# Performance work log

Measured on AMD Instinct MI355X. Metric: run time of the kernel, lower is better.

## Reference

```python
import jax, jax.numpy as jnp
import numpy as np

B, T, D, H, L = 4, 2048, 256, 4, 2
HD = D // H
VOCAB, MAX_BITS, MLP_H = 32, 64, 64


def setup_inputs() -> dict:
    key = jax.random.key(0)
    ks = jax.random.split(key, 20)
    s = 0.02
    n = lambda k, shp: (jax.random.normal(k, shp, jnp.float32) * s)
    inp = {
        'tokens': jax.random.randint(ks[0], (B, T), 0, VOCAB),
        'embed': n(ks[1], (VOCAB, D)),
        'ln1_w': jnp.ones((L, D)), 'ln1_b': jnp.zeros((L, D)),
        'qkv_w': n(ks[2], (L, D, 3 * D)), 'qkv_b': jnp.zeros((L, 3 * D)),
        'proj_w': n(ks[3], (L, D, D)), 'proj_b': jnp.zeros((L, D)),
        'ln2_w': jnp.ones((L, D)), 'ln2_b': jnp.zeros((L, D)),
        'ffn1_w': n(ks[4], (L, D, 4 * D)), 'ffn1_b': jnp.zeros((L, 4 * D)),
        'ffn2_w': n(ks[5], (L, 4 * D, D)), 'ffn2_b': jnp.zeros((L, D)),
        'lnf_w': jnp.ones((D,)), 'lnf_b': jnp.zeros((D,)),
        'out_queries': n(ks[6], (MAX_BITS * 2, D)),
        'outp_w': n(ks[7], (D, 1)), 'outp_b': jnp.zeros((1,)),
        'mlp_w1': n(ks[8], (3, MLP_H)), 'mlp_b1': jnp.zeros((MLP_H,)),
        'mlp_w2': n(ks[9], (MLP_H, MLP_H)), 'mlp_b2': jnp.zeros((MLP_H,)),
        'mlp_w3': n(ks[10], (MLP_H, 2)), 'mlp_b3': jnp.zeros((2,)),
    }
    return inp


def _layernorm(x, w, b, eps=1e-5):
    mu = jnp.mean(x, axis=-1, keepdims=True)
    var = jnp.mean(jnp.square(x - mu), axis=-1, keepdims=True)
    return (x - mu) * jax.lax.rsqrt(var + eps) * w + b


def _rope_tables(t_len, hd):
    inv_freq = 1.0 / (10000.0 ** (jnp.arange(0, hd, 2, dtype=jnp.float32) / hd))
    freqs = jnp.outer(jnp.arange(t_len, dtype=jnp.float32), inv_freq)  # [T, hd/2]
    emb = jnp.concatenate([freqs, freqs], axis=-1)                     # [T, hd]
    return jnp.cos(emb)[None, :, None, :], jnp.sin(emb)[None, :, None, :]


def _rotate_half(x):
    x1, x2 = x[..., : x.shape[-1] // 2], x[..., x.shape[-1] // 2:]
    return jnp.concatenate([-x2, x1], axis=-1)


def _attention(x, qkv_w, qkv_b, proj_w, proj_b):
    b, t, c = x.shape
    qkv = (x @ qkv_w + qkv_b).reshape(b, t, 3, H, HD)
    q, k, v = qkv[:, :, 0], qkv[:, :, 1], qkv[:, :, 2]  # [B,T,H,HD]
    cos, sin = _rope_tables(t, HD)
    q = q * cos + _rotate_half(q) * sin
    k = k * cos + _rotate_half(k) * sin
    scores = jnp.einsum('bthd,bshd->bhts', q, k) / jnp.sqrt(jnp.float32(HD))
    causal = jnp.tril(jnp.ones((t, t), dtype=bool))
    scores = jnp.where(causal, scores, -jnp.inf)
    attn = jax.nn.softmax(scores, axis=-1)
    out = jnp.einsum('bhts,bshd->bthd', attn, v).reshape(b, t, c)
    return out @ proj_w + proj_b


def reference(tokens, embed, ln1_w, ln1_b, qkv_w, qkv_b, proj_w, proj_b,
              ln2_w, ln2_b, ffn1_w, ffn1_b, ffn2_w, ffn2_b, lnf_w, lnf_b,
              out_queries, outp_w, outp_b,
              mlp_w1, mlp_b1, mlp_w2, mlp_b2, mlp_w3, mlp_b3):
    x = embed[tokens]  # [B,T,D]
    for l in range(L):
        x = x + _attention(_layernorm(x, ln1_w[l], ln1_b[l]),
                           qkv_w[l], qkv_b[l], proj_w[l], proj_b[l])
        h = _layernorm(x, ln2_w[l], ln2_b[l])
        h = jax.nn.gelu(h @ ffn1_w[l] + ffn1_b[l], approximate=False)
        x = x + (h @ ffn2_w[l] + ffn2_b[l])
    x = _layernorm(x, lnf_w, lnf_b)
    # query cross-attention for bit-pair selection
    q_scores = jnp.einsum('qd,btd->bqt', out_queries, x) / jnp.sqrt(jnp.float32(D))
    q_attn = jax.nn.softmax(q_scores, axis=-1)           # [B, 2*MAX_BITS, T]
    selected = jnp.einsum('bqt,btd->bqd', q_attn, x)
    bits = jax.nn.sigmoid((selected @ outp_w + outp_b)[..., 0])
    pairs = bits.reshape(-1, MAX_BITS, 2)                # [B, MAX_BITS, 2]

    # sequential full-adder over bits
    def step(carry, ab):  # carry [B], ab [B,2]
        z = jnp.concatenate([ab, carry[:, None]], axis=-1)  # [B,3]
        h = jax.nn.relu(z @ mlp_w1 + mlp_b1)
        h = jax.nn.relu(h @ mlp_w2 + mlp_b2)
        o = jax.nn.sigmoid(h @ mlp_w3 + mlp_b3)
        return o[:, 1], o[:, 0]

    carry0 = jnp.zeros((pairs.shape[0],), jnp.float32)
    carry, sum_bits = jax.lax.scan(step, carry0, jnp.swapaxes(pairs, 0, 1))
    sum_all = jnp.concatenate([sum_bits.T, carry[:, None]], axis=1)  # [B, MAX_BITS+1]
    return sum_all, pairs, q_attn
```

## Files before the change

### kernel.cpp

```cpp
#include <hip/hip_runtime.h>
#include <hip/hip_bf16.h>

#define BB 4
#define TT 2048
#define DD 256
#define HH 4
#define HDD 64
#define NROW 8192
#define NQ 128

typedef __hip_bfloat16 bf16;
typedef __attribute__((ext_vector_type(8))) short bf8v;
typedef __attribute__((ext_vector_type(4))) short bf4v;
typedef __attribute__((ext_vector_type(4))) float f4v;
typedef __attribute__((ext_vector_type(2))) unsigned int u2v;

__device__ __forceinline__ bf16 f2b(float v){ return __float2bfloat16(v); }
__device__ __forceinline__ short f2bs(float v){
    bf16 h = __float2bfloat16(v);
    return *reinterpret_cast<short*>(&h);
}
__device__ __forceinline__ float bs2f(short s){
    bf16 h = *reinterpret_cast<bf16*>(&s);
    return __bfloat162float(h);
}
__device__ __forceinline__ float rl(float v, int l){
    return __uint_as_float(__builtin_amdgcn_readlane(__float_as_uint(v), l));
}

#define DPP_ROR_ADD(v, ctrl) \
    ((v) + __int_as_float(__builtin_amdgcn_update_dpp(0, __float_as_int(v), (ctrl), 0xF, 0xF, false)))
#define DPP_ROR_MAX(v, ctrl) \
    fmaxf((v), __int_as_float(__builtin_amdgcn_update_dpp(0, __float_as_int(v), (ctrl), 0xF, 0xF, false)))

__device__ __forceinline__ void plswap16(float v, float& a, float& b){
#if __has_builtin(__builtin_amdgcn_permlane16_swap)
    u2v r = __builtin_amdgcn_permlane16_swap(__float_as_uint(v), __float_as_uint(v), false, false);
    a = __uint_as_float(r.x); b = __uint_as_float(r.y);
#else
    a = v; b = v;
    asm volatile("" : "+v"(b));
    asm("v_permlane16_swap_b32 %0, %1" : "+v"(a), "+v"(b));
#endif
}
__device__ __forceinline__ void plswap32(float v, float& a, float& b){
#if __has_builtin(__builtin_amdgcn_permlane32_swap)
    u2v r = __builtin_amdgcn_permlane32_swap(__float_as_uint(v), __float_as_uint(v), false, false);
    a = __uint_as_float(r.x); b = __uint_as_float(r.y);
#else
    a = v; b = v;
    asm volatile("" : "+v"(b));
    asm("v_permlane32_swap_b32 %0, %1" : "+v"(a), "+v"(b));
#endif
}
__device__ __forceinline__ float swap16_add(float v){ float a,b; plswap16(v,a,b); return a + b; }
__device__ __forceinline__ float swap32_add(float v){ float a,b; plswap32(v,a,b); return a + b; }
__device__ __forceinline__ float swap16_max(float v){ float a,b; plswap16(v,a,b); return fmaxf(a,b); }
__device__ __forceinline__ float swap32_max(float v){ float a,b; plswap32(v,a,b); return fmaxf(a,b); }
__device__ __forceinline__ float wsum(float v){
    v = DPP_ROR_ADD(v, 0x121); v = DPP_ROR_ADD(v, 0x122);
    v = DPP_ROR_ADD(v, 0x124); v = DPP_ROR_ADD(v, 0x128);
    v = swap16_add(v); v = swap32_add(v);
    return v;
}
__device__ __forceinline__ float wmax(float v){
    v = DPP_ROR_MAX(v, 0x121); v = DPP_ROR_MAX(v, 0x122);
    v = DPP_ROR_MAX(v, 0x124); v = DPP_ROR_MAX(v, 0x128);
    v = swap16_max(v); v = swap32_max(v);
    return v;
}

#define MFMA32(A,B,C) __builtin_amdgcn_mfma_f32_16x16x32_bf16((A),(B),(C),0,0,0)
#if __has_builtin(__builtin_amdgcn_mfma_f32_16x16x16bf16_1k)
#define MFMA16(A,B,C) __builtin_amdgcn_mfma_f32_16x16x16bf16_1k((A),(B),(C),0,0,0)
#else
__device__ __forceinline__ f4v mfma16_asm(bf4v a, bf4v b, f4v c){
    f4v d;
    asm("v_mfma_f32_16x16x16_bf16 %0, %1, %2, %3" : "=v"(d) : "v"(a), "v"(b), "v"(c));
    return d;
}
#define MFMA16(A,B,C) mfma16_asm((A),(B),(C))
#endif

__global__ __launch_bounds__(256) void k_wtall(const float* __restrict__ qkvw,
                                               const float* __restrict__ projw,
                                               const float* __restrict__ f1w,
                                               const float* __restrict__ f2w,
                                               bf16* __restrict__ wt,
                                               const float* __restrict__ oq, bf16* __restrict__ oqb,
                                               float* __restrict__ cosT, float* __restrict__ sinT,
                                               const float* __restrict__ w2, float* __restrict__ w2t,
                                               const int* __restrict__ tok,
                                               const float* __restrict__ emb,
                                               const float* __restrict__ ln1w,
                                               const float* __restrict__ ln1b,
                                               float* __restrict__ x,
                                               bf16* __restrict__ xnb){
    __shared__ float t[32][33];
    int z = blockIdx.z;
    if (z >= 9){
        int bid = blockIdx.y*32 + blockIdx.x;
        int tid = threadIdx.y*32 + threadIdx.x;
        int row = (z-9)*4096 + bid*4 + (tid >> 6);
        int lane = tid & 63;
        f4v v = *(const f4v*)(emb + (long)tok[row]*DD + lane*4);
        *(f4v*)(x + (long)row*DD + lane*4) = v;
        float s  = (v[0]+v[1]) + (v[2]+v[3]);
        float s2 = (v[0]*v[0]+v[1]*v[1]) + (v[2]*v[2]+v[3]*v[3]);
        s = wsum(s); s2 = wsum(s2);
        float mu  = s * (1.0f/DD);
        float var = s2 * (1.0f/DD) - mu*mu;
        float rs  = rsqrtf(var + 1e-5f);
        f4v wv4 = *(const f4v*)(ln1w + lane*4);
        f4v bv4 = *(const f4v*)(ln1b + lane*4);
        bf4v o;
        #pragma unroll
        for (int i=0;i<4;i++) o[i] = f2bs((v[i]-mu)*rs*wv4[i] + bv4[i]);
        *(bf4v*)(xnb + (long)row*DD + lane*4) = o;
        return;
    }
    if (z == 8){
        int bid = blockIdx.y*32 + blockIdx.x;
        if (bid >= 256) return;
        int gid = bid*256 + threadIdx.y*32 + threadIdx.x;
        int tt = gid >> 5, dd = gid & 31;
        float invf = powf(10000.0f, -(float)(2*dd)/64.0f);
        float ang = (float)tt * invf;
        float sn, cs;
        sincosf(ang, &sn, &cs);
        cosT[gid] = cs; sinT[gid] = sn;
        if (gid < NQ*DD) oqb[gid] = f2b(oq[gid]);
        if (gid < 4096){ int j = gid >> 6, k = gid & 63; w2t[gid] = w2[k*64 + j]; }
        return;
    }
    int l = z >> 2, type = z & 3;
    long L = (long)l*786432;
    int K, M; const float* src; long doff;
    if (type == 0){ K=256;  M=768;  src = qkvw + (long)l*256*768;  doff = L; }
    else if (type == 1){ K=256;  M=256;  src = projw + (long)l*256*256; doff = L + 196608; }
    else if (type == 2){ K=256;  M=1024; src = f1w  + (long)l*256*1024; doff = L + 262144; }
    else               { K=1024; M=256;  src = f2w  + (long)l*1024*256; doff = L + 524288; }
    int m0 = blockIdx.x*32, k0 = blockIdx.y*32;
    if (m0 >= M || k0 >= K) return;
    bf16* dst = wt + doff;
    int tx = threadIdx.x, ty = threadIdx.y;
    #pragma unroll
    for (int i=0;i<4;i++)
        t[ty+i*8][tx] = src[(long)(k0+ty+i*8)*M + m0 + tx];
    __syncthreads();
    #pragma unroll
    for (int i=0;i<4;i++)
        dst[(long)(m0+ty+i*8)*K + k0 + tx] = f2b(t[tx][ty+i*8]);
}

__global__ __launch_bounds__(256) void k_lnb(const float* __restrict__ X,
                                             const float* __restrict__ w,
                                             const float* __restrict__ b,
                                             bf16* __restrict__ Y){
    int row = blockIdx.x*4 + (threadIdx.x >> 6);
    int lane = threadIdx.x & 63;
    f4v v = *(const f4v*)(X + (long)row*DD + lane*4);
    float s  = (v[0]+v[1]) + (v[2]+v[3]);
    float s2 = (v[0]*v[0]+v[1]*v[1]) + (v[2]*v[2]+v[3]*v[3]);
    s = wsum(s); s2 = wsum(s2);
    float mu  = s * (1.0f/DD);
    float var = s2 * (1.0f/DD) - mu*mu;
    float rs  = rsqrtf(var + 1e-5f);
    f4v wv4 = *(const f4v*)(w + lane*4);
    f4v bv4 = *(const f4v*)(b + lane*4);
    bf4v o;
    #pragma unroll
    for (int i=0;i<4;i++) o[i] = f2bs((v[i]-mu)*rs*wv4[i] + bv4[i]);
    *(bf4v*)(Y + (long)row*DD + lane*4) = o;
}

__global__ __launch_bounds__(256) void k_lnf(const float* __restrict__ X,
                                             const float* __restrict__ w,
                                             const float* __restrict__ b,
                                             const float* __restrict__ ow,
                                             bf16* __restrict__ Yb,
                                             float* __restrict__ g){
    int row = blockIdx.x*4 + (threadIdx.x >> 6);
    int lane = threadIdx.x & 63;
    f4v v = *(const f4v*)(X + (long)row*DD + lane*4);
    float s  = (v[0]+v[1]) + (v[2]+v[3]);
    float s2 = (v[0]*v[0]+v[1]*v[1]) + (v[2]*v[2]+v[3]*v[3]);
    s = wsum(s); s2 = wsum(s2);
    float mu  = s * (1.0f/DD);
    float var = s2 * (1.0f/DD) - mu*mu;
    float rs  = rsqrtf(var + 1e-5f);
    f4v wv4 = *(const f4v*)(w + lane*4);
    f4v bv4 = *(const f4v*)(b + lane*4);
    f4v ov4 = *(const f4v*)(ow + lane*4);
    bf4v o;
    float gp = 0.f;
    #pragma unroll
    for (int i=0;i<4;i++){
        float y = (v[i]-mu)*rs*wv4[i] + bv4[i];
        o[i] = f2bs(y);
        gp += y * ov4[i];
    }
    *(bf4v*)(Yb + (long)row*DD + lane*4) = o;
    gp = wsum(gp);
    if (lane == 0) g[row] = gp;
}

__global__ __launch_bounds__(256) void k_mgemm(const bf16* __restrict__ A,
                                               const bf16* __restrict__ Wt,
                                               const float* __restrict__ bias,
                                               float* __restrict__ Cf,
                                               bf16* __restrict__ Cb,
                                               int K, int M, int mode){
    __shared__ short As[2][128*64];
    __shared__ short Ws[2][64*64];
    int tid = threadIdx.x;
    int lane = tid & 63, wv = tid >> 6;
    int n0 = blockIdx.y * 128, m0 = blockIdx.x * 64;
    int rbase = (wv >> 1) * 64, cbase = (wv & 1) * 32;
    f4v acc[4][2] = {};
    bf8v va[4], vw[2];
    #pragma unroll
    for (int c=0;c<4;c++){
        int idx = c*256 + tid;
        va[c] = *(const bf8v*)(A + (long)(n0 + (idx>>3))*K + ((idx&7)<<3));
    }
    #pragma unroll
    for (int c=0;c<2;c++){
        int idx = c*256 + tid;
        vw[c] = *(const bf8v*)(Wt + (long)(m0 + (idx>>3))*K + ((idx&7)<<3));
    }
    int buf = 0;
    for (int k0 = 0; k0 < K; k0 += 64){
        #pragma unroll
        for (int c=0;c<4;c++){
            int idx = c*256 + tid, row = idx>>3;
            *(bf8v*)&As[buf][row*64 + (((idx&7)<<3) ^ ((row&7)<<3))] = va[c];
        }
        #pragma unroll
        for (int c=0;c<2;c++){
            int idx = c*256 + tid, row = idx>>3;
            *(bf8v*)&Ws[buf][row*64 + (((idx&7)<<3) ^ ((row&7)<<3))] = vw[c];
        }
        __syncthreads();
        if (k0 + 64 < K){
            #pragma unroll
            for (int c=0;c<4;c++){
                int idx = c*256 + tid;
                va[c] = *(const bf8v*)(A + (long)(n0 + (idx>>3))*K + k0 + 64 + ((idx&7)<<3));
            }
            #pragma unroll
            for (int c=0;c<2;c++){
                int idx = c*256 + tid;
                vw[c] = *(const bf8v*)(Wt + (long)(m0 + (idx>>3))*K + k0 + 64 + ((idx&7)<<3));
            }
        }
        int k8 = (lane >> 4) << 3;
        #pragma unroll
        for (int h=0; h<2; h++){
            bf8v af[4], bfr[2];
            #pragma unroll
            for (int i=0;i<4;i++){
                int row = rbase + i*16 + (lane&15);
                af[i] = *(bf8v*)&As[buf][row*64 + ((h*32 + k8) ^ ((row&7)<<3))];
            }
            #pragma unroll
            for (int j=0;j<2;j++){
                int row = cbase + j*16 + (lane&15);
                bfr[j] = *(bf8v*)&Ws[buf][row*64 + ((h*32 + k8) ^ ((row&7)<<3))];
            }
            #pragma unroll
            for (int i=0;i<4;i++)
                #pragma unroll
                for (int j=0;j<2;j++)
                    acc[i][j] = MFMA32(af[i], bfr[j], acc[i][j]);
        }
        buf ^= 1;
    }
    int rq = (lane >> 4) * 4;
    int cl = lane & 15;
    #pragma unroll
    for (int i=0;i<4;i++){
        #pragma unroll
        for (int j=0;j<2;j++){
            int m = m0 + cbase + j*16 + cl;
            float bs = bias[m];
            #pragma unroll
            for (int r=0;r<4;r++){
                int n = n0 + rbase + i*16 + rq + r;
                float v = acc[i][j][r] + bs;
                long idx = (long)n*M + m;
                if (mode == 0)      Cf[idx] = v;
                else if (mode == 1) Cf[idx] += v;
                else if (mode == 2) Cb[idx] = f2b(0.5f*v*(1.0f + erff(v*0.70710678118654752f)));
                else                Cb[idx] = f2b(v);
            }
        }
    }
}

__global__ __launch_bounds__(256) void k_mgemm64(const bf16* __restrict__ A,
                                                 const bf16* __restrict__ Wt,
                                                 const float* __restrict__ bias,
                                                 float* __restrict__ Cf,
                                                 bf16* __restrict__ Cb,
                                                 int K, int M, int mode){
    __shared__ short As[2][64*64];
    __shared__ short Ws[2][64*64];
    int tid = threadIdx.x;
    int lane = tid & 63, wv = tid >> 6;
    int n0 = blockIdx.y * 64, m0 = blockIdx.x * 64;
    int rbase = (wv >> 1) * 32, cbase = (wv & 1) * 32;
    f4v acc[2][2] = {};
    bf8v va[2], vw[2];
    #pragma unroll
    for (int c=0;c<2;c++){
        int idx = c*256 + tid;
        va[c] = *(const bf8v*)(A  + (long)(n0 + (idx>>3))*K + ((idx&7)<<3));
        vw[c] = *(const bf8v*)(Wt + (long)(m0 + (idx>>3))*K + ((idx&7)<<3));
    }
    int buf = 0;
    for (int k0 = 0; k0 < K; k0 += 64){
        #pragma unroll
        for (int c=0;c<2;c++){
            int idx = c*256 + tid, row = idx>>3;
            *(bf8v*)&As[buf][row*64 + (((idx&7)<<3) ^ ((row&7)<<3))] = va[c];
            *(bf8v*)&Ws[buf][row*64 + (((idx&7)<<3) ^ ((row&7)<<3))] = vw[c];
        }
        __syncthreads();
        if (k0 + 64 < K){
            #pragma unroll
            for (int c=0;c<2;c++){
                int idx = c*256 + tid;
                va[c] = *(const bf8v*)(A  + (long)(n0 + (idx>>3))*K + k0 + 64 + ((idx&7)<<3));
                vw[c] = *(const bf8v*)(Wt + (long)(m0 + (idx>>3))*K + k0 + 64 + ((idx&7)<<3));
            }
        }
        int k8 = (lane >> 4) << 3;
        #pragma unroll
        for (int h=0; h<2; h++){
            bf8v af[2], bfr[2];
            #pragma unroll
            for (int i=0;i<2;i++){
                int row = rbase + i*16 + (lane&15);
                af[i] = *(bf8v*)&As[buf][row*64 + ((h*32 + k8) ^ ((row&7)<<3))];
            }
            #pragma unroll
            for (int j=0;j<2;j++){
                int row = cbase + j*16 + (lane&15);
                bfr[j] = *(bf8v*)&Ws[buf][row*64 + ((h*32 + k8) ^ ((row&7)<<3))];
            }
            #pragma unroll
            for (int i=0;i<2;i++)
                #pragma unroll
                for (int j=0;j<2;j++)
                    acc[i][j] = MFMA32(af[i], bfr[j], acc[i][j]);
        }
        buf ^= 1;
    }
    int rq = (lane >> 4) * 4;
    int cl = lane & 15;
    #pragma unroll
    for (int i=0;i<2;i++){
        #pragma unroll
        for (int j=0;j<2;j++){
            int m = m0 + cbase + j*16 + cl;
            float bs = bias[m];
            #pragma unroll
            for (int r=0;r<4;r++){
                int n = n0 + rbase + i*16 + rq + r;
                float v = acc[i][j][r] + bs;
                long idx = (long)n*M + m;
                if (mode == 0)      Cf[idx] = v;
                else if (mode == 1) Cf[idx] += v;
                else if (mode == 2) Cb[idx] = f2b(0.5f*v*(1.0f + erff(v*0.70710678118654752f)));
                else                Cb[idx] = f2b(v);
            }
        }
    }
}

__global__ __launch_bounds__(256) void k_mgemmQKV(const bf16* __restrict__ A,
                                                  const bf16* __restrict__ Wt,
                                                  const float* __restrict__ bias,
                                                  const float* __restrict__ cosT,
                                                  const float* __restrict__ sinT,
                                                  bf16* __restrict__ qb,
                                                  bf16* __restrict__ kb,
                                                  bf16* __restrict__ vt){
    __shared__ short As[128*64];
    __shared__ short Ws[64*64];
    __shared__ short E[128][68];
    const int K = 256, M = 768;
    int tid = threadIdx.x;
    int lane = tid & 63, wv = tid >> 6;
    int n0 = blockIdx.y * 128, m0 = blockIdx.x * 64;
    int rbase = (wv >> 1) * 64, cbase = (wv & 1) * 32;
    f4v acc[4][2] = {};
    for (int k0 = 0; k0 < K; k0 += 64){
        bf8v va[4], vw[2];
        #pragma unroll
        for (int c=0;c<4;c++){
            int idx = c*256 + tid;
            va[c] = *(const bf8v*)(A + (long)(n0 + (idx>>3))*K + k0 + ((idx&7)<<3));
        }
        #pragma unroll
        for (int c=0;c<2;c++){
            int idx = c*256 + tid;
            vw[c] = *(const bf8v*)(Wt + (long)(m0 + (idx>>3))*K + k0 + ((idx&7)<<3));
        }
        __syncthreads();
        #pragma unroll
        for (int c=0;c<4;c++){
            int idx = c*256 + tid, row = idx>>3;
            *(bf8v*)&As[row*64 + (((idx&7)<<3) ^ ((row&7)<<3))] = va[c];
        }
        #pragma unroll
        for (int c=0;c<2;c++){
            int idx = c*256 + tid, row = idx>>3;
            *(bf8v*)&Ws[row*64 + (((idx&7)<<3) ^ ((row&7)<<3))] = vw[c];
        }
        __syncthreads();
        int k8 = (lane >> 4) << 3;
        #pragma unroll
        for (int h=0; h<2; h++){
            bf8v af[4], bfr[2];
            #pragma unroll
            for (int i=0;i<4;i++){
                int row = rbase + i*16 + (lane&15);
                af[i] = *(bf8v*)&As[row*64 + ((h*32 + k8) ^ ((row&7)<<3))];
            }
            #pragma unroll
            for (int j=0;j<2;j++){
                int row = cbase + j*16 + (lane&15);
                bfr[j] = *(bf8v*)&Ws[row*64 + ((h*32 + k8) ^ ((row&7)<<3))];
            }
            #pragma unroll
            for (int i=0;i<4;i++)
                #pragma unroll
                for (int j=0;j<2;j++)
                    acc[i][j] = MFMA32(af[i], bfr[j], acc[i][j]);
        }
    }
    int rq = (lane >> 4) * 4;
    int cl = lane & 15;
    #pragma unroll
    for (int i=0;i<4;i++){
        #pragma unroll
        for (int j=0;j<2;j++){
            int cc = cbase + j*16 + cl;
            float bs = bias[m0 + cc];
            #pragma unroll
            for (int r=0;r<4;r++)
                E[rbase + i*16 + rq + r][cc] = f2bs(acc[i][j][r] + bs);
        }
    }
    __syncthreads();
    int part = m0 >> 8;
    int h = (m0 >> 6) & 3;
    int b = n0 >> 11;
    int t0 = n0 & 2047;
    int bh = b*HH + h;
    if (part < 2){
        bf16* dst0 = part ? kb : qb;
        int r2 = tid >> 2;
        int c0 = (tid & 3) * 16;
        int cpx = c0 ^ 32;
        #pragma unroll
        for (int half=0; half<2; half++){
            int row = half*64 + r2;
            int t = t0 + row;
            bf8v e0 = *(bf8v*)&E[row][c0];
            bf8v e1 = *(bf8v*)&E[row][c0+8];
            bf8v p0 = *(bf8v*)&E[row][cpx];
            bf8v p1 = *(bf8v*)&E[row][cpx+8];
            const float* ct = cosT + t*32;
            const float* st = sinT + t*32;
            short o[16];
            #pragma unroll
            for (int i=0;i<8;i++){
                int d = c0 + i, dd = d & 31;
                float cs = ct[dd], sn = st[dd];
                float v = bs2f(e0[i]), v2 = bs2f(p0[i]);
                o[i] = f2bs((d < 32) ? (v*cs - v2*sn) : (v*cs + v2*sn));
            }
            #pragma unroll
            for (int i=0;i<8;i++){
                int d = c0 + 8 + i, dd = d & 31;
                float cs = ct[dd], sn = st[dd];
                float v = bs2f(e1[i]), v2 = bs2f(p1[i]);
                o[8+i] = f2bs((d < 32) ? (v*cs - v2*sn) : (v*cs + v2*sn));
            }
            short* dp = (short*)dst0 + ((long)bh*TT + t)*64 + c0;
            *(bf8v*)dp     = *(bf8v*)&o[0];
            *(bf8v*)(dp+8) = *(bf8v*)&o[8];
        }
    } else {
        int tIdx0 = t0 >> 6;
        int d  = (tid & 127) >> 1;
        int k0 = (tid & 1) * 32;
        int tt = tid >> 7;
        short o[32];
        #pragma unroll
        for (int k=0;k<32;k++) o[k] = E[tt*64 + k0 + k][d];
        short* dp = (short*)vt + (((long)bh*32 + tIdx0 + tt)*64 + d)*64 + k0;
        *(bf8v*)dp      = *(bf8v*)&o[0];
        *(bf8v*)(dp+8)  = *(bf8v*)&o[8];
        *(bf8v*)(dp+16) = *(bf8v*)&o[16];
        *(bf8v*)(dp+24) = *(bf8v*)&o[24];
    }
}

__global__ __launch_bounds__(256) void k_fattn(const bf16* __restrict__ qb,
                                               const bf16* __restrict__ kb,
                                               const bf16* __restrict__ vt,
                                               bf16* __restrict__ ob){
    __shared__ short Ks[2][64][72];
    __shared__ short Vs[2][64][68];
    int bh = blockIdx.y;
    int qt = (int)(gridDim.x - 1) - (int)blockIdx.x;
    int tid = threadIdx.x;
    int lane = tid & 63, w = tid >> 6;
    int col = lane & 15, quad = lane >> 4;
    int q0 = qt*64 + w*16;
    const bf16* qp = qb + ((long)bh*TT + q0 + col)*64 + quad*8;
    bf8v bq0 = *(const bf8v*)(qp);
    bf8v bq1 = *(const bf8v*)(qp + 32);
    f4v oc[4] = {};
    float lsum = 0.f;
    int qglob = q0 + col;
    int srow = tid >> 2, sc0 = (tid & 3) * 16;
    const short* kgb = (const short*)kb + ((long)bh*TT + srow)*64 + sc0;
    const short* vgb = (const short*)vt + (((long)bh*32)*64 + srow)*64 + sc0;

    bf8v pk0 = *(const bf8v*)kgb;
    bf8v pk1 = *(const bf8v*)(kgb + 8);
    bf8v pv0 = *(const bf8v*)vgb;
    bf8v pv1 = *(const bf8v*)(vgb + 8);
    *(bf8v*)&Ks[0][srow][sc0]     = pk0;
    *(bf8v*)&Ks[0][srow][sc0 + 8] = pk1;
    *(bf8v*)&Vs[0][srow][sc0]     = pv0;
    *(bf8v*)&Vs[0][srow][sc0 + 8] = pv1;

    int buf = 0;
    for (int kt=0; kt<=qt; kt++){
        __syncthreads();
        bool more = (kt < qt);
        if (more){
            const short* kg = kgb + (long)(kt+1)*4096;
            const short* vg = vgb + (long)(kt+1)*4096;
            pk0 = *(const bf8v*)kg;
            pk1 = *(const bf8v*)(kg + 8);
            pv0 = *(const bf8v*)vg;
            pv1 = *(const bf8v*)(vg + 8);
        }
        bool diag = (kt == qt);
        int ntmax = diag ? w : 3;
        bf4v bp[4];
        #pragma unroll
        for (int nt=0; nt<4; nt++){
            if (nt > ntmax) continue;
            bf8v ka0 = *(const bf8v*)&Ks[buf][nt*16 + col][quad*8];
            bf8v ka1 = *(const bf8v*)&Ks[buf][nt*16 + col][32 + quad*8];
            f4v st = {};
            st = MFMA32(ka0, bq0, st);
            st = MFMA32(ka1, bq1, st);
            int key0 = kt*64 + nt*16 + quad*4;
            bf4v pb;
            #pragma unroll
            for (int r=0; r<4; r++){
                float e = __expf(st[r]*0.125f);
                if (diag && (key0 + r > qglob)) e = 0.f;
                lsum += e;
                pb[r] = f2bs(e);
            }
            bp[nt] = pb;
        }
        #pragma unroll
        for (int dt=0; dt<4; dt++){
            #pragma unroll
            for (int nt=0; nt<4; nt++){
                if (nt > ntmax) continue;
                bf4v va = *(const bf4v*)&Vs[buf][dt*16 + col][nt*16 + quad*4];
                oc[dt] = MFMA16(va, bp[nt], oc[dt]);
            }
        }
        if (more){
            *(bf8v*)&Ks[buf^1][srow][sc0]     = pk0;
            *(bf8v*)&Ks[buf^1][srow][sc0 + 8] = pk1;
            *(bf8v*)&Vs[buf^1][srow][sc0]     = pv0;
            *(bf8v*)&Vs[buf^1][srow][sc0 + 8] = pv1;
        }
        buf ^= 1;
    }
    lsum += __shfl_xor(lsum, 16, 64);
    lsum += __shfl_xor(lsum, 32, 64);
    float linv = 1.0f / lsum;

    int b = bh / HH, h = bh % HH;
    long obase = ((long)b*TT + q0 + col)*DD + h*64 + quad*4;
    #pragma unroll
    for (int dt=0; dt<4; dt++){
        bf4v o4;
        #pragma unroll
        for (int r=0; r<4; r++) o4[r] = f2bs(oc[dt][r]*linv);
        *(bf4v*)(ob + obase + dt*16) = o4;
    }
}

__global__ __launch_bounds__(256) void k_score(const bf16* __restrict__ oqb,
                                               const bf16* __restrict__ xfb,
                                               float* __restrict__ S){
    int b = blockIdx.y, t0 = blockIdx.x*32;
    int tid = threadIdx.x, lane = tid & 63, w = tid >> 6;
    int col = lane & 15, quad = lane >> 4, k8 = quad << 3;
    const bf16* xb = xfb + (long)b*TT*DD;
    f4v acc[2][2] = {};
    #pragma unroll
    for (int ko=0; ko<8; ko++){
        int kk = ko*32 + k8;
        bf8v a0 = *(const bf8v*)(oqb + (long)(w*32 +      col)*DD + kk);
        bf8v a1 = *(const bf8v*)(oqb + (long)(w*32 + 16 + col)*DD + kk);
        #pragma unroll
        for (int bt=0; bt<2; bt++){
            bf8v bv = *(const bf8v*)(xb + (long)(t0 + bt*16 + col)*DD + kk);
            acc[0][bt] = MFMA32(a0, bv, acc[0][bt]);
            acc[1][bt] = MFMA32(a1, bv, acc[1][bt]);
        }
    }
    #pragma unroll
    for (int qt2=0; qt2<2; qt2++){
        #pragma unroll
        for (int bt=0; bt<2; bt++){
            #pragma unroll
            for (int r=0; r<4; r++){
                int q = w*32 + qt2*16 + quad*4 + r;
                S[((long)b*NQ + q)*TT + t0 + bt*16 + col] = acc[qt2][bt][r]*0.0625f;
            }
        }
    }
}

__global__ __launch_bounds__(256) void k_psoft(const float* __restrict__ S,
                                               const float* __restrict__ g,
                                               const float* __restrict__ obias,
                                               float* __restrict__ out_qattn,
                                               float* __restrict__ out_pairs,
                                               float* __restrict__ bits){
    __shared__ float cmax[4], cs[4], cg[4];
    int bq = blockIdx.x, b = bq >> 7;
    int tid = threadIdx.x, wv = tid >> 6, lane = tid & 63;
    const f4v* S4 = (const f4v*)(S + (long)bq*TT);
    f4v s0 = S4[tid], s1 = S4[tid + 256];
    float lmax = fmaxf(fmaxf(fmaxf(s0[0],s0[1]), fmaxf(s0[2],s0[3])),
                       fmaxf(fmaxf(s1[0],s1[1]), fmaxf(s1[2],s1[3])));
    lmax = wmax(lmax);
    if (lane == 0) cmax[wv] = lmax;
    __syncthreads();
    float m = fmaxf(fmaxf(cmax[0],cmax[1]), fmaxf(cmax[2],cmax[3]));
    const f4v* g4 = (const f4v*)(g + (long)b*TT);
    f4v gv0 = g4[tid], gv1 = g4[tid + 256];
    f4v e0, e1;
    #pragma unroll
    for (int i=0;i<4;i++){ e0[i] = __expf(s0[i]-m); e1[i] = __expf(s1[i]-m); }
    float lsum = (e0[0]+e0[1]+e0[2]+e0[3]) + (e1[0]+e1[1]+e1[2]+e1[3]);
    float gdot = (e0[0]*gv0[0]+e0[1]*gv0[1]+e0[2]*gv0[2]+e0[3]*gv0[3])
               + (e1[0]*gv1[0]+e1[1]*gv1[1]+e1[2]*gv1[2]+e1[3]*gv1[3]);
    lsum = wsum(lsum); gdot = wsum(gdot);
    if (lane == 0){ cs[wv] = lsum; cg[wv] = gdot; }
    __syncthreads();
    float Lr = (cs[0]+cs[1]) + (cs[2]+cs[3]);
    float G  = (cg[0]+cg[1]) + (cg[2]+cg[3]);
    float inv = 1.0f / Lr;
    f4v* out4 = (f4v*)(out_qattn + (long)bq*TT);
    out4[tid]       = e0 * inv;
    out4[tid + 256] = e1 * inv;
    if (tid == 0){
        float bit = 1.0f/(1.0f + expf(-(G*inv + obias[0])));
        bits[bq] = bit;
        out_pairs[bq] = bit;
    }
}

__global__ __launch_bounds__(64) void k_scan(const float* __restrict__ bits,
                                             const float* __restrict__ w1, const float* __restrict__ b1,
                                             const float* __restrict__ w2t, const float* __restrict__ b2,
                                             const float* __restrict__ w3, const float* __restrict__ b3,
                                             float* __restrict__ out_sum){
    __shared__ __align__(16) float h1s[2][64];
    int b = blockIdx.x, lane = threadIdx.x;
    float w1c0 = w1[lane], w1c1 = w1[64 + lane], w1c2 = w1[128 + lane];
    float b1v = b1[lane], b2v = b2[lane];
    float w3c0 = w3[lane*2 + 0], w3c1 = w3[lane*2 + 1];
    float b30 = b3[0], b31 = b3[1];
    const f4v* wrow = (const f4v*)(w2t + (long)lane*64);
    f4v c0v = wrow[0],  c1v = wrow[1],  c2v = wrow[2],  c3v = wrow[3],
        c4v = wrow[4],  c5v = wrow[5],  c6v = wrow[6],  c7v = wrow[7],
        c8v = wrow[8],  c9v = wrow[9],  cav = wrow[10], cbv = wrow[11],
        ccv = wrow[12], cdv = wrow[13], cev = wrow[14], cfv = wrow[15];
    float z0v = bits[b*128 + lane*2 + 0];
    float z1v = bits[b*128 + lane*2 + 1];
    float carry = 0.f;
    float a1 = rl(z0v, 0)*w1c0 + rl(z1v, 0)*w1c1 + b1v;
    for (int step=0; step<64; step++){
        float h1 = fmaxf(carry*w1c2 + a1, 0.f);
        float* hb = h1s[step & 1];
        hb[lane] = h1;
        __syncthreads();
        if (step < 63){
            a1 = rl(z0v, step+1)*w1c0 + rl(z1v, step+1)*w1c1 + b1v;
        }
        const f4v* hv = (const f4v*)hb;
        f4v va = hv[0]*c0v,  vb = hv[1]*c1v,  vc = hv[2]*c2v,   vd = hv[3]*c3v;
        va += hv[4]*c4v;   vb += hv[5]*c5v;   vc += hv[6]*c6v;   vd += hv[7]*c7v;
        va += hv[8]*c8v;   vb += hv[9]*c9v;   vc += hv[10]*cav;  vd += hv[11]*cbv;
        va += hv[12]*ccv;  vb += hv[13]*cdv;  vc += hv[14]*cev;  vd += hv[15]*cfv;
        f4v vs = (va + vb) + (vc + vd);
        float h2 = fmaxf(((vs[0] + vs[1]) + (vs[2] + vs[3])) + b2v, 0.f);
        float t0 = h2*w3c0, t1 = h2*w3c1;
        t0 = DPP_ROR_ADD(t0, 0x121); t1 = DPP_ROR_ADD(t1, 0x121);
        t0 = DPP_ROR_ADD(t0, 0x122); t1 = DPP_ROR_ADD(t1, 0x122);
        t0 = DPP_ROR_ADD(t0, 0x124); t1 = DPP_ROR_ADD(t1, 0x124);
        t0 = DPP_ROR_ADD(t0, 0x128); t1 = DPP_ROR_ADD(t1, 0x128);
        t0 = swap16_add(t0); t1 = swap16_add(t1);
        t0 = swap32_add(t0); t1 = swap32_add(t1);
        float o0 = 1.0f/(1.0f + __expf(-(t0 + b30)));
        carry    = 1.0f/(1.0f + __expf(-(t1 + b31)));
        if (lane == 0) out_sum[b*65 + step] = o0;
    }
    if (lane == 0) out_sum[b*65 + 64] = carry;
}

extern "C" void kernel_launch(void* const* d_in, const int* in_sizes, int n_in,
                              void* d_out, int out_size, void* d_ws, size_t ws_size,
                              hipStream_t stream){
    const int*   tok   = (const int*)d_in[0];
    const float* emb   = (const float*)d_in[1];
    const float* ln1w  = (const float*)d_in[2];
    const float* ln1b  = (const float*)d_in[3];
    const float* qkvw  = (const float*)d_in[4];
    const float* qkvb  = (const float*)d_in[5];
    const float* projw = (const float*)d_in[6];
    const float* projb = (const float*)d_in[7];
    const float* ln2w  = (const float*)d_in[8];
    const float* ln2b  = (const float*)d_in[9];
    const float* f1w   = (const float*)d_in[10];
    const float* f1b   = (const float*)d_in[11];
    const float* f2w   = (const float*)d_in[12];
    const float* f2bb  = (const float*)d_in[13];
    const float* lnfw  = (const float*)d_in[14];
    const float* lnfb  = (const float*)d_in[15];
    const float* oq    = (const float*)d_in[16];
    const float* ow    = (const float*)d_in[17];
    const float* obias = (const float*)d_in[18];
    const float* w1    = (const float*)d_in[19];
    const float* b1    = (const float*)d_in[20];
    const float* w2    = (const float*)d_in[21];
    const float* b2    = (const float*)d_in[22];
    const float* w3    = (const float*)d_in[23];
    const float* b3    = (const float*)d_in[24];
    float* out = (float*)d_out;

    const long MB = 1048576;
    char* W = (char*)d_ws;
    float* x     = (float*)(W);
    bf16*  attnb = (bf16*)(W + 8*MB);
    bf16*  hb    = (bf16*)(W + 16*MB);
    bf16*  qb    = (bf16*)(W + 32*MB);
    bf16*  kb    = (bf16*)(W + 36*MB);
    bf16*  vt    = (bf16*)(W + 44*MB);
    bf16*  xnb   = (bf16*)(W + 48*MB);
    bf16*  wt    = (bf16*)(W + 52*MB);
    float* bits  = (float*)(W + 55*MB);
    bf16*  oqb   = (bf16*)(W + 56*MB);
    float* cosT  = (float*)(W + 57*MB);
    float* sinT  = cosT + 65536;
    float* w2t   = (float*)(W + 58*MB);
    bf16*  xfb   = (bf16*)(W + 32*MB);
    float* g     = (float*)(W + 36*MB);
    float* S     = (float*)(W + 40*MB);

    k_wtall<<<dim3(32, 32, 11), dim3(32,8), 0, stream>>>(qkvw, projw, f1w, f2w, wt,
                                                         oq, oqb, cosT, sinT, w2, w2t,
                                                         tok, emb, ln1w, ln1b, x, xnb);

    for (int l=0; l<2; l++){
        long L = (long)l*786432;
        if (l) k_lnb<<<NROW/4, 256, 0, stream>>>(x, ln1w + l*DD, ln1b + l*DD, xnb);
        k_mgemmQKV<<<dim3(768/64, 64), 256, 0, stream>>>(
            xnb, wt + L, qkvb + l*768, cosT, sinT, qb, kb, vt);
        k_fattn<<<dim3(TT/64, BB*HH), 256, 0, stream>>>(qb, kb, vt, attnb);
        k_mgemm64<<<dim3(256/64, NROW/64), 256, 0, stream>>>(
            attnb, wt + L + 196608, projb + l*DD, x, (bf16*)0, 256, 256, 1);
        k_lnb<<<NROW/4, 256, 0, stream>>>(x, ln2w + l*DD, ln2b + l*DD, xnb);
        k_mgemm<<<dim3(1024/64, 64), 256, 0, stream>>>(
            xnb, wt + L + 262144, f1b + l*1024, (float*)0, hb, 256, 1024, 2);
        k_mgemm64<<<dim3(256/64, NROW/64), 256, 0, stream>>>(
            hb, wt + L + 524288, f2bb + l*DD, x, (bf16*)0, 1024, 256, 1);
    }
    k_lnf<<<NROW/4, 256, 0, stream>>>(x, lnfw, lnfb, ow, xfb, g);
    k_score<<<dim3(TT/32, BB), 256, 0, stream>>>(oqb, xfb, S);
    k_psoft<<<BB*NQ, 256, 0, stream>>>(S, g, obias, out + 772, out + 260, bits);
    k_scan<<<4, 64, 0, stream>>>(bits, w1, b1, w2t, b2, w3, b3, out);
}
```

Baseline: 357.1 us.

## Split causal attention KV range across two blocks and combine partials

The flash attention kernel now splits each query tile's key range into two halves processed by separate blocks (grid z=2). Each block writes unnormalized fp32 partial outputs and row sums, and a new combine kernel adds them and normalizes to bf16. This shortens the longest per-block causal loop and adds parallelism. The cost is extra global traffic for the fp32 partials and one additional launch.

```diff
diff --git a/kernel.cpp b/kernel.cpp
--- a/kernel.cpp
+++ b/kernel.cpp
@@ -513,10 +513,12 @@
 __global__ __launch_bounds__(256) void k_fattn(const bf16* __restrict__ qb,
                                                const bf16* __restrict__ kb,
                                                const bf16* __restrict__ vt,
-                                               bf16* __restrict__ ob){
+                                               float* __restrict__ Opart,
+                                               float* __restrict__ lsumP){
     __shared__ short Ks[2][64][72];
     __shared__ short Vs[2][64][68];
     int bh = blockIdx.y;
+    int z  = blockIdx.z;
     int qt = (int)(gridDim.x - 1) - (int)blockIdx.x;
     int tid = threadIdx.x;
     int lane = tid & 63, w = tid >> 6;
@@ -532,79 +534,102 @@
     const short* kgb = (const short*)kb + ((long)bh*TT + srow)*64 + sc0;
     const short* vgb = (const short*)vt + (((long)bh*32)*64 + srow)*64 + sc0;
 
-    bf8v pk0 = *(const bf8v*)kgb;
-    bf8v pk1 = *(const bf8v*)(kgb + 8);
-    bf8v pv0 = *(const bf8v*)vgb;
-    bf8v pv1 = *(const bf8v*)(vgb + 8);
-    *(bf8v*)&Ks[0][srow][sc0]     = pk0;
-    *(bf8v*)&Ks[0][srow][sc0 + 8] = pk1;
-    *(bf8v*)&Vs[0][srow][sc0]     = pv0;
-    *(bf8v*)&Vs[0][srow][sc0 + 8] = pv1;
-
-    int buf = 0;
-    for (int kt=0; kt<=qt; kt++){
-        __syncthreads();
-        bool more = (kt < qt);
-        if (more){
-            const short* kg = kgb + (long)(kt+1)*4096;
-            const short* vg = vgb + (long)(kt+1)*4096;
-            pk0 = *(const bf8v*)kg;
-            pk1 = *(const bf8v*)(kg + 8);
-            pv0 = *(const bf8v*)vg;
-            pv1 = *(const bf8v*)(vg + 8);
-        }
-        bool diag = (kt == qt);
-        int ntmax = diag ? w : 3;
-        bf4v bp[4];
-        #pragma unroll
-        for (int nt=0; nt<4; nt++){
-            if (nt > ntmax) continue;
-            bf8v ka0 = *(const bf8v*)&Ks[buf][nt*16 + col][quad*8];
-            bf8v ka1 = *(const bf8v*)&Ks[buf][nt*16 + col][32 + quad*8];
-            f4v st = {};
-            st = MFMA32(ka0, bq0, st);
-            st = MFMA32(ka1, bq1, st);
-            int key0 = kt*64 + nt*16 + quad*4;
-            bf4v pb;
-            #pragma unroll
-            for (int r=0; r<4; r++){
-                float e = __expf(st[r]*0.125f);
-                if (diag && (key0 + r > qglob)) e = 0.f;
-                lsum += e;
-                pb[r] = f2bs(e);
-            }
-            bp[nt] = pb;
-        }
-        #pragma unroll
-        for (int dt=0; dt<4; dt++){
+    int ntot = qt + 1;
+    int h0   = (ntot + 1) >> 1;
+    int kt0  = z ? h0 : 0;
+    int kt1  = z ? ntot : h0;
+
+    if (kt0 < kt1){
+        bf8v pk0 = *(const bf8v*)(kgb + (long)kt0*4096);
+        bf8v pk1 = *(const bf8v*)(kgb + (long)kt0*4096 + 8);
+        bf8v pv0 = *(const bf8v*)(vgb + (long)kt0*4096);
+        bf8v pv1 = *(const bf8v*)(vgb + (long)kt0*4096 + 8);
+        *(bf8v*)&Ks[0][srow][sc0]     = pk0;
+        *(bf8v*)&Ks[0][srow][sc0 + 8] = pk1;
+        *(bf8v*)&Vs[0][srow][sc0]     = pv0;
+        *(bf8v*)&Vs[0][srow][sc0 + 8] = pv1;
+
+        int buf = 0;
+        for (int kt=kt0; kt<kt1; kt++){
+            __syncthreads();
+            bool more = (kt + 1 < kt1);
+            if (more){
+                const short* kg = kgb + (long)(kt+1)*4096;
+                const short* vg = vgb + (long)(kt+1)*4096;
+                pk0 = *(const bf8v*)kg;
+                pk1 = *(const bf8v*)(kg + 8);
+                pv0 = *(const bf8v*)vg;
+                pv1 = *(const bf8v*)(vg + 8);
+            }
+            bool diag = (kt == qt);
+            int ntmax = diag ? w : 3;
+            bf4v bp[4];
             #pragma unroll
             for (int nt=0; nt<4; nt++){
                 if (nt > ntmax) continue;
-                bf4v va = *(const bf4v*)&Vs[buf][dt*16 + col][nt*16 + quad*4];
-                oc[dt] = MFMA16(va, bp[nt], oc[dt]);
-            }
-        }
-        if (more){
-            *(bf8v*)&Ks[buf^1][srow][sc0]     = pk0;
-            *(bf8v*)&Ks[buf^1][srow][sc0 + 8] = pk1;
-            *(bf8v*)&Vs[buf^1][srow][sc0]     = pv0;
-            *(bf8v*)&Vs[buf^1][srow][sc0 + 8] = pv1;
-        }
-        buf ^= 1;
+                bf8v ka0 = *(const bf8v*)&Ks[buf][nt*16 + col][quad*8];
+                bf8v ka1 = *(const bf8v*)&Ks[buf][nt*16 + col][32 + quad*8];
+                f4v st = {};
+                st = MFMA32(ka0, bq0, st);
+                st = MFMA32(ka1, bq1, st);
+                int key0 = kt*64 + nt*16 + quad*4;
+                bf4v pb;
+                #pragma unroll
+                for (int r=0; r<4; r++){
+                    float e = __expf(st[r]*0.125f);
+                    if (diag && (key0 + r > qglob)) e = 0.f;
+                    lsum += e;
+                    pb[r] = f2bs(e);
+                }
+                bp[nt] = pb;
+            }
+            #pragma unroll
+            for (int dt=0; dt<4; dt++){
+                #pragma unroll
+                for (int nt=0; nt<4; nt++){
+                    if (nt > ntmax) continue;
+                    bf4v va = *(const bf4v*)&Vs[buf][dt*16 + col][nt*16 + quad*4];
+                    oc[dt] = MFMA16(va, bp[nt], oc[dt]);
+                }
+            }
+            if (more){
+                *(bf8v*)&Ks[buf^1][srow][sc0]     = pk0;
+                *(bf8v*)&Ks[buf^1][srow][sc0 + 8] = pk1;
+                *(bf8v*)&Vs[buf^1][srow][sc0]     = pv0;
+                *(bf8v*)&Vs[buf^1][srow][sc0 + 8] = pv1;
+            }
+            buf ^= 1;
+        }
     }
     lsum += __shfl_xor(lsum, 16, 64);
     lsum += __shfl_xor(lsum, 32, 64);
-    float linv = 1.0f / lsum;
 
     int b = bh / HH, h = bh % HH;
     long obase = ((long)b*TT + q0 + col)*DD + h*64 + quad*4;
-    #pragma unroll
-    for (int dt=0; dt<4; dt++){
-        bf4v o4;
-        #pragma unroll
-        for (int r=0; r<4; r++) o4[r] = f2bs(oc[dt][r]*linv);
-        *(bf4v*)(ob + obase + dt*16) = o4;
-    }
+    float* Op = Opart + (long)z*2097152;
+    #pragma unroll
+    for (int dt=0; dt<4; dt++)
+        *(f4v*)(Op + obase + dt*16) = oc[dt];
+    if (quad == 0)
+        lsumP[(long)z*32768 + (long)bh*TT + q0 + col] = lsum;
+}
+
+__global__ __launch_bounds__(256) void k_fcomb(const float* __restrict__ Opart,
+                                               const float* __restrict__ lsumP,
+                                               bf16* __restrict__ ob){
+    int row = blockIdx.x*4 + (threadIdx.x >> 6);
+    int lane = threadIdx.x & 63;
+    int b = row >> 11, t = row & 2047;
+    int hh = lane >> 4;
+    long base = (long)row*DD + lane*4;
+    f4v o0 = *(const f4v*)(Opart + base);
+    f4v o1 = *(const f4v*)(Opart + 2097152 + base);
+    long li = (long)(b*HH + hh)*TT + t;
+    float inv = 1.0f / (lsumP[li] + lsumP[32768 + li]);
+    bf4v o;
+    #pragma unroll
+    for (int i=0;i<4;i++) o[i] = f2bs((o0[i]+o1[i])*inv);
+    *(bf4v*)(ob + base) = o;
 }
 
 __global__ __launch_bounds__(256) void k_score(const bf16* __restrict__ oqb,
@@ -765,12 +790,14 @@
     float* x     = (float*)(W);
     bf16*  attnb = (bf16*)(W + 8*MB);
     bf16*  hb    = (bf16*)(W + 16*MB);
+    float* Opart = (float*)(W + 16*MB);
     bf16*  qb    = (bf16*)(W + 32*MB);
     bf16*  kb    = (bf16*)(W + 36*MB);
     bf16*  vt    = (bf16*)(W + 44*MB);
     bf16*  xnb   = (bf16*)(W + 48*MB);
     bf16*  wt    = (bf16*)(W + 52*MB);
     float* bits  = (float*)(W + 55*MB);
+    float* lsumP = (float*)(W + 55*MB + 524288);
     bf16*  oqb   = (bf16*)(W + 56*MB);
     float* cosT  = (float*)(W + 57*MB);
     float* sinT  = cosT + 65536;
@@ -788,7 +815,8 @@
         if (l) k_lnb<<<NROW/4, 256, 0, stream>>>(x, ln1w + l*DD, ln1b + l*DD, xnb);
         k_mgemmQKV<<<dim3(768/64, 64), 256, 0, stream>>>(
             xnb, wt + L, qkvb + l*768, cosT, sinT, qb, kb, vt);
-        k_fattn<<<dim3(TT/64, BB*HH), 256, 0, stream>>>(qb, kb, vt, attnb);
+        k_fattn<<<dim3(TT/64, BB*HH, 2), 256, 0, stream>>>(qb, kb, vt, Opart, lsumP);
+        k_fcomb<<<NROW/4, 256, 0, stream>>>(Opart, lsumP, attnb);
         k_mgemm64<<<dim3(256/64, NROW/64), 256, 0, stream>>>(
             attnb, wt + L + 196608, projb + l*DD, x, (bf16*)0, 256, 256, 1);
         k_lnb<<<NROW/4, 256, 0, stream>>>(x, ln2w + l*DD, ln2b + l*DD, xnb);
```

Measured after the change: 371.6 us. 1.04x slower.
